# Kernel optimization log

Measured on AMD Instinct MI355X. Metric: run time of the kernel, lower is better.

Reference implementation:

```python
import jax, jax.numpy as jnp
import numpy as np

B, N = 4, 128
INPUT_SIZE, Z_SIZE = 512, 256
D_TENSOR, N_HEADS, SEQ_LEN = 64, 8, 64
D = D_TENSOR * N_HEADS * SEQ_LEN  # 32768


def setup_inputs() -> dict:
    key = jax.random.key(0)
    ks = jax.random.split(key, 10)
    s = lambda fan_in: 1.0 / np.sqrt(fan_in)
    return {
        "x": jax.random.normal(ks[0], (B, N, INPUT_SIZE), dtype=jnp.float32),
        "z": jax.random.normal(ks[1], (B, N, Z_SIZE), dtype=jnp.float32),
        "Wq": jax.random.uniform(ks[2], (Z_SIZE, D), jnp.float32, -s(Z_SIZE), s(Z_SIZE)),
        "bq": jax.random.uniform(ks[3], (D,), jnp.float32, -s(Z_SIZE), s(Z_SIZE)),
        "Wk": jax.random.uniform(ks[4], (INPUT_SIZE, D), jnp.float32, -s(INPUT_SIZE), s(INPUT_SIZE)),
        "bk": jax.random.uniform(ks[5], (D,), jnp.float32, -s(INPUT_SIZE), s(INPUT_SIZE)),
        "Wv": jax.random.uniform(ks[6], (INPUT_SIZE, D), jnp.float32, -s(INPUT_SIZE), s(INPUT_SIZE)),
        "bv": jax.random.uniform(ks[7], (D,), jnp.float32, -s(INPUT_SIZE), s(INPUT_SIZE)),
        "Wo": jax.random.uniform(ks[8], (D, INPUT_SIZE), jnp.float32, -s(D), s(D)),
        "bo": jax.random.uniform(ks[9], (INPUT_SIZE,), jnp.float32, -s(D), s(D)),
    }


def reference(x, z, Wq, bq, Wk, bk, Wv, bv, Wo, bo):
    # Q, K, V: [B, N, heads, seq_len, d_tensor]
    Q = (z @ Wq + bq).reshape(B, N, N_HEADS, SEQ_LEN, D_TENSOR)
    K = (x @ Wk + bk).reshape(B, N, N_HEADS, SEQ_LEN, D_TENSOR)
    V = (x @ Wv + bv).reshape(B, N, N_HEADS, SEQ_LEN, D_TENSOR)
    scores = jnp.einsum("bnhqd,bnhkd->bnhqk", Q, K) / np.sqrt(D_TENSOR).astype(np.float32)
    attn = jax.nn.softmax(scores, axis=-1)
    out = jnp.einsum("bnhqk,bnhkd->bnhqd", attn, V).reshape(B, N, D)
    return out @ Wo + bo
```

## Files before the change

### kernel.cpp

```cpp
#include <hip/hip_runtime.h>
#include <stdint.h>


typedef __attribute__((ext_vector_type(8))) short short8;
typedef __attribute__((ext_vector_type(4))) float floatx4;

__device__ __forceinline__ unsigned short f2bf(float f) {
  union { float f; unsigned int u; } v; v.f = f;
  unsigned int u = v.u + 0x7FFFu + ((v.u >> 16) & 1u);
  return (unsigned short)(u >> 16);
}

__device__ __forceinline__ unsigned int cvt_pk_bf16(float lo, float hi) {
  unsigned int r;
  asm("v_cvt_pk_bf16_f32 %0, %1, %2" : "=v"(r) : "v"(lo), "v"(hi));
  return r;
}

#define MFMA16(a, b, c) __builtin_amdgcn_mfma_f32_16x16x32_bf16((a), (b), (c), 0, 0, 0)

#define STAGE_TILE(SRC, LD, LDSARR)                                            \
  do {                                                                         \
    _Pragma("unroll") for (int i_ = 0; i_ < 4; ++i_) {                         \
      int e_ = tid + (i_ << 8);                                                \
      int r_ = e_ >> 3;                                                        \
      int c_ = (e_ & 7) ^ (r_ & 7);                                            \
      __builtin_amdgcn_global_load_lds(                                        \
          (const __attribute__((address_space(1))) unsigned int*)((SRC) +      \
              (size_t)r_ * (LD) + (c_ << 3)),                                  \
          (__attribute__((address_space(3))) unsigned int*)(&(LDSARR)[e_ << 3]),\
          16, 0, 0);                                                           \
    }                                                                          \
  } while (0)

#define FRAG(LDSARR, ROW, KS)                                                  \
  (*(const short8*)(&(LDSARR)[(((ROW) << 6)) +                                 \
      ((((((KS) << 2) + quad)) ^ ((ROW) & 7)) << 3)]))

template <int LDW>
__device__ __forceinline__ void stage_b_f32(const float* __restrict__ Wp,
                                            unsigned short* Bs, int tid) {
  const int n = tid & 127;
  const int octb = __builtin_amdgcn_readfirstlane(tid >> 7);
#pragma unroll
  for (int g = 0; g < 4; ++g) {
    const int oct = octb + 2 * g;
    const float* src = Wp + (size_t)(oct << 3) * LDW + n;
    float f[8];
#pragma unroll
    for (int j = 0; j < 8; ++j) f[j] = src[(size_t)j * LDW];
    uint4 p;
    p.x = cvt_pk_bf16(f[0], f[1]);
    p.y = cvt_pk_bf16(f[2], f[3]);
    p.z = cvt_pk_bf16(f[4], f[5]);
    p.w = cvt_pk_bf16(f[6], f[7]);
    *(uint4*)(&Bs[(n << 6) + ((oct ^ (n & 7)) << 3)]) = p;
  }
}

__global__ __launch_bounds__(256) void convert_xz(const float* __restrict__ x,
                                                  const float* __restrict__ z,
                                                  unsigned short* __restrict__ xb,
                                                  unsigned short* __restrict__ zb) {
  int idx = (blockIdx.x * 256 + threadIdx.x) * 8;
  const float* src;
  unsigned short* dst;
  if (idx < 262144) { src = x + idx; dst = xb + idx; }
  else              { src = z + (idx - 262144); dst = zb + (idx - 262144); }
  float4 f0 = *(const float4*)src;
  float4 f1 = *(const float4*)(src + 4);
  uint4 p;
  p.x = f2bf(f0.x) | ((unsigned)f2bf(f0.y) << 16);
  p.y = f2bf(f0.z) | ((unsigned)f2bf(f0.w) << 16);
  p.z = f2bf(f1.x) | ((unsigned)f2bf(f1.y) << 16);
  p.w = f2bf(f1.z) | ((unsigned)f2bf(f1.w) << 16);
  *(uint4*)dst = p;
}

__global__ __launch_bounds__(256, 2) void gemm_qkv(const unsigned short* __restrict__ xb,
                                                   const unsigned short* __restrict__ zb,
                                                   const float* __restrict__ Wq,
                                                   const float* __restrict__ Wk,
                                                   const float* __restrict__ Wv,
                                                   const float* __restrict__ bq,
                                                   const float* __restrict__ bk,
                                                   const float* __restrict__ bv,
                                                   unsigned short* __restrict__ Qb,
                                                   unsigned short* __restrict__ Kb,
                                                   unsigned short* __restrict__ Vb) {
  __shared__ __align__(16) unsigned short As[128 * 64];
  __shared__ __align__(16) unsigned short Bs[128 * 64];
  const int tid = threadIdx.x;
  const int zsel = blockIdx.z;
  const unsigned short* A;
  const float* W;
  const float* bias;
  unsigned short* C;
  int Ka;
  if (zsel == 0)      { A = zb; W = Wq; bias = bq; C = Qb; Ka = 256; }
  else if (zsel == 1) { A = xb; W = Wk; bias = bk; C = Kb; Ka = 512; }
  else                { A = xb; W = Wv; bias = bv; C = Vb; Ka = 512; }
  const int id = blockIdx.x;
  const int xcd = id & 7, bj = id >> 3;
  const int m0 = (bj & 3) << 7;
  const int n0 = ((xcd << 5) | (bj >> 2)) << 7;
  const int lane = tid & 63, wid = tid >> 6;
  const int quad = lane >> 4, l15 = lane & 15;
  const int wm = wid >> 1, wn = wid & 1;
  floatx4 acc[4][4] = {};
  for (int k0 = 0; k0 < Ka; k0 += 64) {
    STAGE_TILE(A + (size_t)m0 * Ka + k0, Ka, As);
    stage_b_f32<32768>(W + (size_t)k0 * 32768 + n0, Bs, tid);
    __syncthreads();
#pragma unroll
    for (int ks = 0; ks < 2; ++ks) {
      short8 aF[4], bF[4];
#pragma unroll
      for (int mi = 0; mi < 4; ++mi) aF[mi] = FRAG(As, wm * 64 + mi * 16 + l15, ks);
#pragma unroll
      for (int ni = 0; ni < 4; ++ni) bF[ni] = FRAG(Bs, wn * 64 + ni * 16 + l15, ks);
#pragma unroll
      for (int mi = 0; mi < 4; ++mi)
#pragma unroll
        for (int ni = 0; ni < 4; ++ni)
          acc[mi][ni] = MFMA16(aF[mi], bF[ni], acc[mi][ni]);
    }
    __syncthreads();
  }
#pragma unroll
  for (int ni = 0; ni < 4; ++ni) {
    int col = n0 + wn * 64 + ni * 16 + l15;
    float bv2 = bias[col];
#pragma unroll
    for (int mi = 0; mi < 4; ++mi) {
      int row = m0 + wm * 64 + mi * 16 + (quad << 2);
#pragma unroll
      for (int r = 0; r < 4; ++r)
        C[(size_t)(row + r) * 32768 + col] = f2bf(acc[mi][ni][r] + bv2);
    }
  }
}

__global__ __launch_bounds__(256) void attn64(const unsigned short* __restrict__ Qb,
                                              const unsigned short* __restrict__ Kb,
                                              const unsigned short* __restrict__ Vb,
                                              unsigned short* __restrict__ Ob) {
  __shared__ __align__(16) unsigned short Qs[64 * 72];
  __shared__ __align__(16) unsigned short Ks[64 * 72];
  __shared__ __align__(16) unsigned short VT[64 * 72];
  __shared__ __align__(16) unsigned short Ps[64 * 72];
  const int tid = threadIdx.x;
  const int bn = blockIdx.x >> 3, h = blockIdx.x & 7;
  const size_t base = (size_t)bn * 32768 + (size_t)h * 4096;
  const unsigned short* q = Qb + base;
  const unsigned short* k = Kb + base;
  const unsigned short* v = Vb + base;
#pragma unroll
  for (int i = 0; i < 2; ++i) {
    int e = tid + (i << 8);
    int r = e >> 3, dblk = e & 7;
    *(uint4*)(&Qs[r * 72 + dblk * 8]) = *(const uint4*)(q + r * 64 + dblk * 8);
    *(uint4*)(&Ks[r * 72 + dblk * 8]) = *(const uint4*)(k + r * 64 + dblk * 8);
    uint4 vv = *(const uint4*)(v + r * 64 + dblk * 8);
    const unsigned short* pv = (const unsigned short*)&vv;
#pragma unroll
    for (int j = 0; j < 8; ++j)
      VT[(dblk * 8 + j) * 72 + r] = pv[j];
  }
  __syncthreads();
  const int lane = tid & 63, wid = tid >> 6;
  const int quad = lane >> 4, l15 = lane & 15;
  const int qs = wid << 4;
  short8 aq0 = *(const short8*)(&Qs[(qs + l15) * 72 + quad * 8]);
  short8 aq1 = *(const short8*)(&Qs[(qs + l15) * 72 + 32 + quad * 8]);
  floatx4 s[4] = {};
#pragma unroll
  for (int ni = 0; ni < 4; ++ni) {
    short8 b0 = *(const short8*)(&Ks[(ni * 16 + l15) * 72 + quad * 8]);
    short8 b1 = *(const short8*)(&Ks[(ni * 16 + l15) * 72 + 32 + quad * 8]);
    s[ni] = MFMA16(aq0, b0, s[ni]);
    s[ni] = MFMA16(aq1, b1, s[ni]);
  }
#pragma unroll
  for (int r = 0; r < 4; ++r) {
    float e0 = s[0][r] * 0.125f, e1 = s[1][r] * 0.125f;
    float e2 = s[2][r] * 0.125f, e3 = s[3][r] * 0.125f;
    float m = fmaxf(fmaxf(e0, e1), fmaxf(e2, e3));
    m = fmaxf(m, __shfl_xor(m, 1));
    m = fmaxf(m, __shfl_xor(m, 2));
    m = fmaxf(m, __shfl_xor(m, 4));
    m = fmaxf(m, __shfl_xor(m, 8));
    float x0 = __expf(e0 - m), x1 = __expf(e1 - m);
    float x2 = __expf(e2 - m), x3 = __expf(e3 - m);
    float t = x0 + x1 + x2 + x3;
    t += __shfl_xor(t, 1); t += __shfl_xor(t, 2);
    t += __shfl_xor(t, 4); t += __shfl_xor(t, 8);
    float inv = __builtin_amdgcn_rcpf(t);
    int row = qs + (quad << 2) + r;
    Ps[row * 72 +      l15] = f2bf(x0 * inv);
    Ps[row * 72 + 16 + l15] = f2bf(x1 * inv);
    Ps[row * 72 + 32 + l15] = f2bf(x2 * inv);
    Ps[row * 72 + 48 + l15] = f2bf(x3 * inv);
  }
  __syncthreads();
  short8 ap0 = *(const short8*)(&Ps[(qs + l15) * 72 + quad * 8]);
  short8 ap1 = *(const short8*)(&Ps[(qs + l15) * 72 + 32 + quad * 8]);
  floatx4 o[4] = {};
#pragma unroll
  for (int ni = 0; ni < 4; ++ni) {
    short8 b0 = *(const short8*)(&VT[(ni * 16 + l15) * 72 + quad * 8]);
    short8 b1 = *(const short8*)(&VT[(ni * 16 + l15) * 72 + 32 + quad * 8]);
    o[ni] = MFMA16(ap0, b0, o[ni]);
    o[ni] = MFMA16(ap1, b1, o[ni]);
  }
  unsigned short* outp = Ob + base;
#pragma unroll
  for (int ni = 0; ni < 4; ++ni)
#pragma unroll
    for (int r = 0; r < 4; ++r)
      outp[(qs + (quad << 2) + r) * 64 + ni * 16 + l15] = f2bf(o[ni][r]);
}

__global__ __launch_bounds__(256, 2) void gemm_out(const unsigned short* __restrict__ A,
                                                   const float* __restrict__ Wo,
                                                   const float* __restrict__ bias,
                                                   float* __restrict__ C) {
  __shared__ __align__(16) unsigned short As[128 * 64];
  __shared__ __align__(16) unsigned short Bs[128 * 64];
  const int tid = threadIdx.x;
  const int id = blockIdx.x;
  const int xcd = id & 7, bj = id >> 3;
  const int m0 = (bj & 3) << 7;
  const int q = bj >> 2;
  const int n0 = (q & 3) << 7;
  const int ks = (xcd << 2) | (q >> 2);
  const int kbase = ks << 10;
  const int lane = tid & 63, wid = tid >> 6;
  const int quad = lane >> 4, l15 = lane & 15;
  const int wm = wid >> 1, wn = wid & 1;
  floatx4 acc[4][4] = {};
  for (int k0 = kbase; k0 < kbase + 1024; k0 += 64) {
    STAGE_TILE(A + (size_t)m0 * 32768 + k0, 32768, As);
    stage_b_f32<512>(Wo + (size_t)k0 * 512 + n0, Bs, tid);
    __syncthreads();
#pragma unroll
    for (int kss = 0; kss < 2; ++kss) {
      short8 aF[4], bF[4];
#pragma unroll
      for (int mi = 0; mi < 4; ++mi) aF[mi] = FRAG(As, wm * 64 + mi * 16 + l15, kss);
#pragma unroll
      for (int ni = 0; ni < 4; ++ni) bF[ni] = FRAG(Bs, wn * 64 + ni * 16 + l15, kss);
#pragma unroll
      for (int mi = 0; mi < 4; ++mi)
#pragma unroll
        for (int ni = 0; ni < 4; ++ni)
          acc[mi][ni] = MFMA16(aF[mi], bF[ni], acc[mi][ni]);
    }
    __syncthreads();
  }
#pragma unroll
  for (int ni = 0; ni < 4; ++ni) {
    int col = n0 + wn * 64 + ni * 16 + l15;
    float bv0 = (ks == 0) ? bias[col] : 0.0f;
#pragma unroll
    for (int mi = 0; mi < 4; ++mi) {
      int row = m0 + wm * 64 + mi * 16 + (quad << 2);
#pragma unroll
      for (int r = 0; r < 4; ++r)
        atomicAdd(&C[(size_t)(row + r) * 512 + col], acc[mi][ni][r] + bv0);
    }
  }
}

extern "C" void kernel_launch(void* const* d_in, const int* in_sizes, int n_in,
                              void* d_out, int out_size, void* d_ws, size_t ws_size,
                              hipStream_t stream) {
  const float* x  = (const float*)d_in[0];
  const float* z  = (const float*)d_in[1];
  const float* Wq = (const float*)d_in[2];
  const float* bq = (const float*)d_in[3];
  const float* Wk = (const float*)d_in[4];
  const float* bk = (const float*)d_in[5];
  const float* Wv = (const float*)d_in[6];
  const float* bv = (const float*)d_in[7];
  const float* Wo = (const float*)d_in[8];
  const float* bo = (const float*)d_in[9];
  float* out = (float*)d_out;
  char* ws = (char*)d_ws;

  unsigned short* Qb = (unsigned short*)(ws + 0);
  unsigned short* Kb = (unsigned short*)(ws + 33554432);
  unsigned short* Vb = (unsigned short*)(ws + 67108864);
  unsigned short* Ob = (unsigned short*)(ws + 100663296);
  unsigned short* xb = (unsigned short*)(ws + 134217728);
  unsigned short* zb = (unsigned short*)(ws + 134217728 + 524288);

  convert_xz<<<dim3(192), 256, 0, stream>>>(x, z, xb, zb);

  gemm_qkv<<<dim3(1024, 1, 3), 256, 0, stream>>>(xb, zb, Wq, Wk, Wv,
                                                 bq, bk, bv, Qb, Kb, Vb);

  attn64<<<dim3(4096), 256, 0, stream>>>(Qb, Kb, Vb, Ob);

  hipMemsetAsync(d_out, 0, (size_t)out_size * sizeof(float), stream);
  gemm_out<<<dim3(512), 256, 0, stream>>>(Ob, Wo, bo, out);
}
```

Baseline: 378.1 us.

## Double-buffer GEMM tiles with register prefetch and replace atomics with split-K reduce

Both the QKV GEMM and the output GEMM now double-buffer the LDS tiles. The next A tile is loaded directly into LDS and the next fp32 weight tile is prefetched into registers while the current tile is computed, which drops one barrier per k-step. The output GEMM writes per-split partial sums to a workspace instead of issuing atomic adds, and a new reduce kernel sums the 32 partials and adds the bias, removing the memset. In exchange the kernels use more LDS and more registers (32 extra floats), which can lower occupancy, and the partials add an extra 32 MB of workspace traffic.

```diff
diff --git a/kernel.cpp b/kernel.cpp
--- a/kernel.cpp
+++ b/kernel.cpp
@@ -38,22 +38,27 @@
       ((((((KS) << 2) + quad)) ^ ((ROW) & 7)) << 3)]))
 
 template <int LDW>
-__device__ __forceinline__ void stage_b_f32(const float* __restrict__ Wp,
-                                            unsigned short* Bs, int tid) {
-  const int n = tid & 127;
-  const int octb = __builtin_amdgcn_readfirstlane(tid >> 7);
+__device__ __forceinline__ void b_issue(const float* __restrict__ Wp,
+                                        float* fB, int n, int octb) {
 #pragma unroll
   for (int g = 0; g < 4; ++g) {
     const int oct = octb + 2 * g;
     const float* src = Wp + (size_t)(oct << 3) * LDW + n;
-    float f[8];
-#pragma unroll
-    for (int j = 0; j < 8; ++j) f[j] = src[(size_t)j * LDW];
+#pragma unroll
+    for (int j = 0; j < 8; ++j) fB[g * 8 + j] = src[(size_t)j * LDW];
+  }
+}
+
+__device__ __forceinline__ void b_write(unsigned short* Bs, const float* fB,
+                                        int n, int octb) {
+#pragma unroll
+  for (int g = 0; g < 4; ++g) {
+    const int oct = octb + 2 * g;
     uint4 p;
-    p.x = cvt_pk_bf16(f[0], f[1]);
-    p.y = cvt_pk_bf16(f[2], f[3]);
-    p.z = cvt_pk_bf16(f[4], f[5]);
-    p.w = cvt_pk_bf16(f[6], f[7]);
+    p.x = cvt_pk_bf16(fB[g * 8 + 0], fB[g * 8 + 1]);
+    p.y = cvt_pk_bf16(fB[g * 8 + 2], fB[g * 8 + 3]);
+    p.z = cvt_pk_bf16(fB[g * 8 + 4], fB[g * 8 + 5]);
+    p.w = cvt_pk_bf16(fB[g * 8 + 6], fB[g * 8 + 7]);
     *(uint4*)(&Bs[(n << 6) + ((oct ^ (n & 7)) << 3)]) = p;
   }
 }
@@ -88,8 +93,8 @@
                                                    unsigned short* __restrict__ Qb,
                                                    unsigned short* __restrict__ Kb,
                                                    unsigned short* __restrict__ Vb) {
-  __shared__ __align__(16) unsigned short As[128 * 64];
-  __shared__ __align__(16) unsigned short Bs[128 * 64];
+  __shared__ __align__(16) unsigned short As[2][128 * 64];
+  __shared__ __align__(16) unsigned short Bs[2][128 * 64];
   const int tid = threadIdx.x;
   const int zsel = blockIdx.z;
   const unsigned short* A;
@@ -107,25 +112,37 @@
   const int lane = tid & 63, wid = tid >> 6;
   const int quad = lane >> 4, l15 = lane & 15;
   const int wm = wid >> 1, wn = wid & 1;
+  const int n = tid & 127;
+  const int octb = __builtin_amdgcn_readfirstlane(tid >> 7);
+  const int nsteps = Ka >> 6;
+
+  float fB[32];
   floatx4 acc[4][4] = {};
-  for (int k0 = 0; k0 < Ka; k0 += 64) {
-    STAGE_TILE(A + (size_t)m0 * Ka + k0, Ka, As);
-    stage_b_f32<32768>(W + (size_t)k0 * 32768 + n0, Bs, tid);
+  int c = 0;
+  STAGE_TILE(A + (size_t)m0 * Ka, Ka, As[0]);
+  b_issue<32768>(W + n0, fB, n, octb);
+  for (int t = 0; t < nsteps; ++t) {
+    b_write(Bs[c], fB, n, octb);
     __syncthreads();
+    if (t + 1 < nsteps) {
+      STAGE_TILE(A + (size_t)m0 * Ka + ((t + 1) << 6), Ka, As[c ^ 1]);
+      b_issue<32768>(W + ((size_t)(t + 1) << 6) * 32768 + n0, fB, n, octb);
+    }
+    __builtin_amdgcn_sched_barrier(0);
 #pragma unroll
     for (int ks = 0; ks < 2; ++ks) {
       short8 aF[4], bF[4];
 #pragma unroll
-      for (int mi = 0; mi < 4; ++mi) aF[mi] = FRAG(As, wm * 64 + mi * 16 + l15, ks);
-#pragma unroll
-      for (int ni = 0; ni < 4; ++ni) bF[ni] = FRAG(Bs, wn * 64 + ni * 16 + l15, ks);
+      for (int mi = 0; mi < 4; ++mi) aF[mi] = FRAG(As[c], wm * 64 + mi * 16 + l15, ks);
+#pragma unroll
+      for (int ni = 0; ni < 4; ++ni) bF[ni] = FRAG(Bs[c], wn * 64 + ni * 16 + l15, ks);
 #pragma unroll
       for (int mi = 0; mi < 4; ++mi)
 #pragma unroll
         for (int ni = 0; ni < 4; ++ni)
           acc[mi][ni] = MFMA16(aF[mi], bF[ni], acc[mi][ni]);
     }
-    __syncthreads();
+    c ^= 1;
   }
 #pragma unroll
   for (int ni = 0; ni < 4; ++ni) {
@@ -223,10 +240,9 @@
 
 __global__ __launch_bounds__(256, 2) void gemm_out(const unsigned short* __restrict__ A,
                                                    const float* __restrict__ Wo,
-                                                   const float* __restrict__ bias,
-                                                   float* __restrict__ C) {
-  __shared__ __align__(16) unsigned short As[128 * 64];
-  __shared__ __align__(16) unsigned short Bs[128 * 64];
+                                                   float* __restrict__ Cp) {
+  __shared__ __align__(16) unsigned short As[2][128 * 64];
+  __shared__ __align__(16) unsigned short Bs[2][128 * 64];
   const int tid = threadIdx.x;
   const int id = blockIdx.x;
   const int xcd = id & 7, bj = id >> 3;
@@ -238,38 +254,59 @@
   const int lane = tid & 63, wid = tid >> 6;
   const int quad = lane >> 4, l15 = lane & 15;
   const int wm = wid >> 1, wn = wid & 1;
+  const int n = tid & 127;
+  const int octb = __builtin_amdgcn_readfirstlane(tid >> 7);
+
+  float fB[32];
   floatx4 acc[4][4] = {};
-  for (int k0 = kbase; k0 < kbase + 1024; k0 += 64) {
-    STAGE_TILE(A + (size_t)m0 * 32768 + k0, 32768, As);
-    stage_b_f32<512>(Wo + (size_t)k0 * 512 + n0, Bs, tid);
+  int c = 0;
+  STAGE_TILE(A + (size_t)m0 * 32768 + kbase, 32768, As[0]);
+  b_issue<512>(Wo + (size_t)kbase * 512 + n0, fB, n, octb);
+  for (int t = 0; t < 16; ++t) {
+    b_write(Bs[c], fB, n, octb);
     __syncthreads();
+    if (t + 1 < 16) {
+      STAGE_TILE(A + (size_t)m0 * 32768 + kbase + ((t + 1) << 6), 32768, As[c ^ 1]);
+      b_issue<512>(Wo + (size_t)(kbase + ((t + 1) << 6)) * 512 + n0, fB, n, octb);
+    }
+    __builtin_amdgcn_sched_barrier(0);
 #pragma unroll
     for (int kss = 0; kss < 2; ++kss) {
       short8 aF[4], bF[4];
 #pragma unroll
-      for (int mi = 0; mi < 4; ++mi) aF[mi] = FRAG(As, wm * 64 + mi * 16 + l15, kss);
-#pragma unroll
-      for (int ni = 0; ni < 4; ++ni) bF[ni] = FRAG(Bs, wn * 64 + ni * 16 + l15, kss);
+      for (int mi = 0; mi < 4; ++mi) aF[mi] = FRAG(As[c], wm * 64 + mi * 16 + l15, kss);
+#pragma unroll
+      for (int ni = 0; ni < 4; ++ni) bF[ni] = FRAG(Bs[c], wn * 64 + ni * 16 + l15, kss);
 #pragma unroll
       for (int mi = 0; mi < 4; ++mi)
 #pragma unroll
         for (int ni = 0; ni < 4; ++ni)
           acc[mi][ni] = MFMA16(aF[mi], bF[ni], acc[mi][ni]);
     }
-    __syncthreads();
-  }
+    c ^= 1;
+  }
+  float* outp = Cp + (size_t)ks * 262144;
 #pragma unroll
   for (int ni = 0; ni < 4; ++ni) {
     int col = n0 + wn * 64 + ni * 16 + l15;
-    float bv0 = (ks == 0) ? bias[col] : 0.0f;
 #pragma unroll
     for (int mi = 0; mi < 4; ++mi) {
       int row = m0 + wm * 64 + mi * 16 + (quad << 2);
 #pragma unroll
       for (int r = 0; r < 4; ++r)
-        atomicAdd(&C[(size_t)(row + r) * 512 + col], acc[mi][ni][r] + bv0);
-    }
-  }
+        outp[(size_t)(row + r) * 512 + col] = acc[mi][ni][r];
+    }
+  }
+}
+
+__global__ __launch_bounds__(256) void reduce_out(const float* __restrict__ Cp,
+                                                  const float* __restrict__ bias,
+                                                  float* __restrict__ C) {
+  int idx = blockIdx.x * 256 + threadIdx.x;
+  float s = bias[idx & 511];
+#pragma unroll
+  for (int k = 0; k < 32; ++k) s += Cp[(size_t)k * 262144 + idx];
+  C[idx] = s;
 }
 
 extern "C" void kernel_launch(void* const* d_in, const int* in_sizes, int n_in,
@@ -293,7 +330,8 @@
   unsigned short* Vb = (unsigned short*)(ws + 67108864);
   unsigned short* Ob = (unsigned short*)(ws + 100663296);
   unsigned short* xb = (unsigned short*)(ws + 134217728);
-  unsigned short* zb = (unsigned short*)(ws + 134217728 + 524288);
+  unsigned short* zb = (unsigned short*)(ws + 134742016);
+  float*          Cp = (float*)(ws + 135266304);
 
   convert_xz<<<dim3(192), 256, 0, stream>>>(x, z, xb, zb);
 
@@ -302,6 +340,7 @@
 
   attn64<<<dim3(4096), 256, 0, stream>>>(Qb, Kb, Vb, Ob);
 
-  hipMemsetAsync(d_out, 0, (size_t)out_size * sizeof(float), stream);
-  gemm_out<<<dim3(512), 256, 0, stream>>>(Ob, Wo, bo, out);
-}
+  gemm_out<<<dim3(512), 256, 0, stream>>>(Ob, Wo, Cp);
+
+  reduce_out<<<dim3(1024), 256, 0, stream>>>(Cp, bo, out);
+}
```

New measurement: 350.3 us. 7.4% less time.
